# Performance work log

Hardware: AMD Instinct MI355X
Metric: run time of the kernel (lower is better)

Reference implementation:

```python
import jax, jax.numpy as jnp
import numpy as np

IN, H, OUT = 128, 256, 128


def setup_inputs() -> dict:
    key = jax.random.key(0)
    ks = jax.random.split(key, 12)
    B, T = 32, 128
    s_in = 1.0 / np.sqrt(IN)
    s_h = 1.0 / np.sqrt(H)
    return {
        "x": jax.random.normal(ks[0], (B, T, IN), dtype=jnp.float32),
        "timespans": jax.random.uniform(ks[1], (B, T), dtype=jnp.float32),
        "tau_sys": jax.random.uniform(ks[2], (H,), dtype=jnp.float32) * 10.0 + 1.0,
        "sigma": jnp.ones((H,), dtype=jnp.float32) * 0.5,
        "W_A": jax.random.normal(ks[3], (H, H), dtype=jnp.float32) * s_h,
        "W_B": jax.random.normal(ks[4], (H, IN), dtype=jnp.float32) * s_in,
        "b_B": jax.random.normal(ks[5], (H,), dtype=jnp.float32) * s_in,
        "W_C": jax.random.normal(ks[6], (OUT, H), dtype=jnp.float32) * s_h,
        "b_C": jax.random.normal(ks[7], (OUT,), dtype=jnp.float32) * s_h,
        "W_ih": jax.random.normal(ks[8], (4 * H, IN), dtype=jnp.float32) * s_h,
        "W_hh": jax.random.normal(ks[9], (4 * H, H), dtype=jnp.float32) * s_h,
        "b_ih": jax.random.normal(ks[10], (4 * H,), dtype=jnp.float32) * s_h,
        "b_hh": jax.random.normal(ks[11], (4 * H,), dtype=jnp.float32) * s_h,
    }


def _lstm(x, W_ih, W_hh, b_ih, b_hh):
    # x: [B,T,IN] -> backbone_out: [B,T,H]; torch gate order i,f,g,o
    B = x.shape[0]
    xg = jnp.einsum("bti,gi->btg", x, W_ih) + b_ih  # precompute input contribution

    def step(carry, xg_t):
        h, c = carry
        gates = xg_t + h @ W_hh.T + b_hh
        i, f, g, o = jnp.split(gates, 4, axis=-1)
        c = jax.nn.sigmoid(f) * c + jax.nn.sigmoid(i) * jnp.tanh(g)
        h = jax.nn.sigmoid(o) * jnp.tanh(c)
        return (h, c), h

    h0 = jnp.zeros((B, H), dtype=x.dtype)
    c0 = jnp.zeros((B, H), dtype=x.dtype)
    _, hs = jax.lax.scan(step, (h0, c0), jnp.swapaxes(xg, 0, 1))
    return jnp.swapaxes(hs, 0, 1)  # [B,T,H]


def reference(x, timespans, tau_sys, sigma, W_A, W_B, b_B, W_C, b_C,
              W_ih, W_hh, b_ih, b_hh):
    B, T, _ = x.shape
    backbone_out = _lstm(x, W_ih, W_hh, b_ih, b_hh)  # [B,T,H]

    A_eff = W_A / tau_sys[None, :]        # [H,H] (divide columns, as in torch)
    I = jnp.eye(H, dtype=x.dtype)
    Bx = jnp.einsum("bti,hi->bth", x, W_B) + b_B  # precompute B(x_t) for all t

    def step(h, inp):
        x_t_Bx, bb_t, ts_t = inp  # [B,H], [B,H], [B]
        f_h = jnp.tanh(h / sigma)
        At = A_eff[None, :, :] * ts_t[:, None, None]            # [B,H,H]
        exp_At = I + At + 0.5 * jnp.einsum("bij,bjk->bik", At, At)
        h_new = jnp.einsum("bij,bj->bi", exp_At, h)
        drive = x_t_Bx + f_h @ W_A.T
        h_new = h_new + ts_t[:, None] * drive / tau_sys[None, :]
        h_new = h_new + bb_t
        y = h_new @ W_C.T + b_C
        return h_new, y

    h0 = jnp.zeros((B, H), dtype=x.dtype)
    xs = (jnp.swapaxes(Bx, 0, 1), jnp.swapaxes(backbone_out, 0, 1),
          jnp.swapaxes(timespans, 0, 1))
    _, ys = jax.lax.scan(step, h0, xs)
    return jnp.swapaxes(ys, 0, 1)  # [B,T,OUT]
```

## Files before the change

### kernel.cpp

```cpp
#include <hip/hip_runtime.h>
#include <math.h>

#define T_ 128

#define OFF_M2      0
#define OFF_WCOMBT  65536
#define OFF_BIAS    229376
#define OFF_WCT     230656
#define OFF_XG2     263424
#define OFF_BX2     4457728
#define OFF_HSEQ    5506304
#define OFF_HCSEQ   6554880

#define SENTB 0xFFFFFFFFu

typedef float f4 __attribute__((ext_vector_type(4)));

__device__ __forceinline__ float sigm_f(float x) { return 1.0f / (1.0f + __expf(-x)); }
__device__ __forceinline__ float tanh_f(float x) { return 1.0f - 2.0f / (__expf(2.0f * x) + 1.0f); }

__device__ __forceinline__ unsigned long long aload_u64(const unsigned long long* p) {
  return __hip_atomic_load(p, __ATOMIC_RELAXED, __HIP_MEMORY_SCOPE_AGENT);
}
__device__ __forceinline__ void astore_f(float* p, float v) {
  __hip_atomic_store(p, v, __ATOMIC_RELAXED, __HIP_MEMORY_SCOPE_AGENT);
}
__device__ __forceinline__ bool bad_u64(unsigned long long v) {
  return (unsigned)v == SENTB || (unsigned)(v >> 32) == SENTB;
}

__global__ __launch_bounds__(256) void prep_kernel(
    const float* __restrict__ W_ih, const float* __restrict__ W_B,
    const float* __restrict__ b_ih, const float* __restrict__ b_hh,
    const float* __restrict__ b_B,  const float* __restrict__ W_C,
    const float* __restrict__ W_A,  const float* __restrict__ tau,
    float* __restrict__ ws) {
  __shared__ float adrow[256];
  const int blk = blockIdx.x, tid = threadIdx.x;
  if (blk < 640) {
    const int idx = blk * 256 + tid;
    const int k = idx / 1280, c = idx - k * 1280;
    ws[OFF_WCOMBT + idx] = (c < 1024) ? W_ih[c * 128 + k] : W_B[(c - 1024) * 128 + k];
  } else if (blk == 640) {
#pragma unroll
    for (int i = 0; i < 5; ++i) {
      const int id = i * 256 + tid;
      ws[OFF_BIAS + id] = (id < 1024) ? (b_ih[id] + b_hh[id]) : b_B[id - 1024];
    }
  } else if (blk < 769) {
    const int idx = (blk - 641) * 256 + tid;
    const int k = idx >> 7, o = idx & 127;
    ws[OFF_WCT + idx] = W_C[o * 256 + k];
  } else if (blk < 1025) {
    const int i = blk - 769, k = tid;
    const float itk = 1.0f / tau[k];
    adrow[k] = W_A[i * 256 + k] * itk;
    __syncthreads();
    float s = 0.f;
#pragma unroll 8
    for (int m = 0; m < 256; ++m)
      s = fmaf(adrow[m], W_A[m * 256 + k], s);
    ws[OFF_M2 + i * 256 + k] = s * itk;
  } else {
    uint4* dst = (uint4*)(ws + OFF_HSEQ);
    const uint4 sv = make_uint4(SENTB, SENTB, SENTB, SENTB);
    const int tg = (blk - 1025) * 256 + tid;
#pragma unroll
    for (int i = 0; i < 16; ++i) dst[tg + i * 32768] = sv;
  }
}

__global__ __launch_bounds__(256) void xgt_kernel(
    const float* __restrict__ x, const float* __restrict__ WT,
    const float* __restrict__ bias, float* __restrict__ xg2,
    float* __restrict__ bx2) {
  __shared__ float xs[32 * 128];
  const int tid = threadIdx.x;
  const int rt = blockIdx.x, ct = blockIdx.y;
  {
    const float4* src4 = (const float4*)(x + (size_t)rt * 4096);
    float4* d4 = (float4*)xs;
#pragma unroll
    for (int v = 0; v < 4; ++v) d4[v * 256 + tid] = src4[v * 256 + tid];
  }
  __syncthreads();
  const int rg = tid >> 5, cg = tid & 31;
  const int c0 = ct * 256 + cg * 8;
  const float4* b4 = (const float4*)(bias + c0);
  const float4 bA = b4[0], bB = b4[1];
  float a[4][8];
#pragma unroll
  for (int i = 0; i < 4; ++i) {
    a[i][0] = bA.x; a[i][1] = bA.y; a[i][2] = bA.z; a[i][3] = bA.w;
    a[i][4] = bB.x; a[i][5] = bB.y; a[i][6] = bB.z; a[i][7] = bB.w;
  }
  const float4* xr0 = (const float4*)(xs + (rg * 4 + 0) * 128);
  const float4* xr1 = (const float4*)(xs + (rg * 4 + 1) * 128);
  const float4* xr2 = (const float4*)(xs + (rg * 4 + 2) * 128);
  const float4* xr3 = (const float4*)(xs + (rg * 4 + 3) * 128);
#pragma unroll 2
  for (int k4 = 0; k4 < 32; ++k4) {
    const float4 xv0 = xr0[k4], xv1 = xr1[k4], xv2 = xr2[k4], xv3 = xr3[k4];
    const float xk[4][4] = {
        {xv0.x, xv0.y, xv0.z, xv0.w}, {xv1.x, xv1.y, xv1.z, xv1.w},
        {xv2.x, xv2.y, xv2.z, xv2.w}, {xv3.x, xv3.y, xv3.z, xv3.w}};
#pragma unroll
    for (int kk = 0; kk < 4; ++kk) {
      const float4* wp = (const float4*)(WT + (k4 * 4 + kk) * 1280 + c0);
      const float4 wA = wp[0], wB = wp[1];
      const float wv[8] = {wA.x, wA.y, wA.z, wA.w, wB.x, wB.y, wB.z, wB.w};
#pragma unroll
      for (int i = 0; i < 4; ++i)
#pragma unroll
        for (int j = 0; j < 8; ++j)
          a[i][j] = fmaf(wv[j], xk[i][kk], a[i][j]);
    }
  }
#pragma unroll
  for (int i = 0; i < 4; ++i) {
    const int row = rt * 32 + rg * 4 + i;
    const int b = row >> 7, t = row & 127;
    float* dst = (ct < 4)
        ? xg2 + (size_t)(t * 32 + b) * 1024 + ct * 256 + cg * 8
        : bx2 + (size_t)(t * 32 + b) * 256 + cg * 8;
    float4* d4 = (float4*)dst;
    d4[0] = make_float4(a[i][0], a[i][1], a[i][2], a[i][3]);
    d4[1] = make_float4(a[i][4], a[i][5], a[i][6], a[i][7]);
  }
}

__device__ __forceinline__ float wc_elem(
    const float* __restrict__ W_A, const float* __restrict__ M2,
    const float* __restrict__ tau, int ci, float it_i, int kp) {
  if (kp < 256)      return W_A[ci * 256 + kp] / tau[kp];
  else if (kp < 512) return W_A[ci * 256 + (kp - 256)] * it_i;
  else               return 0.5f * M2[ci * 256 + (kp - 512)];
}

__global__ __launch_bounds__(256, 4) void recur_bp_kernel(
    const float* __restrict__ ts_all, const float* __restrict__ tau,
    const float* __restrict__ sigma, const float* __restrict__ W_hh,
    const float* __restrict__ W_A, const float* __restrict__ M2,
    const float* __restrict__ xg2, const float* __restrict__ bx2,
    float* __restrict__ hseq, float* __restrict__ hcseq,
    const float* __restrict__ WCT, const float* __restrict__ bC,
    float* __restrict__ y) {
  const int tid = threadIdx.x;
  const int lane = tid & 63, w = tid >> 6;
  const unsigned long long* hsq  = (const unsigned long long*)hseq;
  const unsigned long long* hcsq = (const unsigned long long*)hcseq;

  __shared__ float h_s[2][256];
  __shared__ float q_s[2][768];

  if (blockIdx.x < 512) {
    const int b = blockIdx.x >> 4, cb16 = blockIdx.x & 15;
    const int kq = lane & 3;
    const int gt = (lane >> 2) & 3;
    const int dim = cb16 * 16 + 4 * w + (lane >> 4);
    const int grow = gt * 256 + dim;
    const f4* wsrc = (const f4*)(W_hh + grow * 256);
    f4 wq0  = wsrc[0 * 4 + kq],  wq1  = wsrc[1 * 4 + kq];
    f4 wq2  = wsrc[2 * 4 + kq],  wq3  = wsrc[3 * 4 + kq];
    f4 wq4  = wsrc[4 * 4 + kq],  wq5  = wsrc[5 * 4 + kq];
    f4 wq6  = wsrc[6 * 4 + kq],  wq7  = wsrc[7 * 4 + kq];
    f4 wq8  = wsrc[8 * 4 + kq],  wq9  = wsrc[9 * 4 + kq];
    f4 wq10 = wsrc[10 * 4 + kq], wq11 = wsrc[11 * 4 + kq];
    f4 wq12 = wsrc[12 * 4 + kq], wq13 = wsrc[13 * 4 + kq];
    f4 wq14 = wsrc[14 * 4 + kq], wq15 = wsrc[15 * 4 + kq];
    asm volatile("" : "+v"(wq0), "+v"(wq1), "+v"(wq2), "+v"(wq3),
                      "+v"(wq4), "+v"(wq5), "+v"(wq6), "+v"(wq7),
                      "+v"(wq8), "+v"(wq9), "+v"(wq10), "+v"(wq11),
                      "+v"(wq12), "+v"(wq13), "+v"(wq14), "+v"(wq15));
    float c_reg = 0.f;
    const int dcol = dim;

    for (int t = 0; t < T_; ++t) {
      const int buf = t & 1;
      float xgi = 0.f, xgf = 0.f, xgg = 0.f, xgo = 0.f;
      if ((lane & 15) == 0) {
        const float* xp = xg2 + (size_t)(t * 32 + b) * 1024 + dcol;
        xgi = xp[0]; xgf = xp[256]; xgg = xp[512]; xgo = xp[768];
      }
      if (t == 0) {
        if (tid < 128) ((float2*)h_s[0])[tid] = make_float2(0.f, 0.f);
      } else if (tid < 128) {
        const unsigned long long* pp = hsq + (size_t)((t - 1) * 32 + b) * 128 + tid;
        unsigned long long v = aload_u64(pp);
        int spins = 0;
        while (bad_u64(v)) {
          if (++spins > 16) __builtin_amdgcn_s_sleep(1);
          v = aload_u64(pp);
        }
        union { unsigned long long u; float2 f; } H; H.u = v;
        ((float2*)h_s[buf])[tid] = H.f;
      }
      __syncthreads();

      const f4* h4 = (const f4*)h_s[buf];
      float s = 0.f;
#define LSTEP(i4, W)                                                         \
      {                                                                      \
        const f4 hv = h4[i4 * 4 + kq];                                       \
        s = fmaf(W.x, hv.x, s); s = fmaf(W.y, hv.y, s);                      \
        s = fmaf(W.z, hv.z, s); s = fmaf(W.w, hv.w, s);                      \
      }
      LSTEP(0, wq0)   LSTEP(1, wq1)   LSTEP(2, wq2)   LSTEP(3, wq3)
      LSTEP(4, wq4)   LSTEP(5, wq5)   LSTEP(6, wq6)   LSTEP(7, wq7)
      LSTEP(8, wq8)   LSTEP(9, wq9)   LSTEP(10, wq10) LSTEP(11, wq11)
      LSTEP(12, wq12) LSTEP(13, wq13) LSTEP(14, wq14) LSTEP(15, wq15)
#undef LSTEP
      s += __shfl_xor(s, 1); s += __shfl_xor(s, 2);
      const int base = lane & 48;
      const float gi = __shfl(s, base);
      const float gf = __shfl(s, base + 4);
      const float gg = __shfl(s, base + 8);
      const float go = __shfl(s, base + 12);
      if ((lane & 15) == 0) {
        const float i_ = sigm_f(gi + xgi);
        const float f_ = sigm_f(gf + xgf);
        const float g_ = tanh_f(gg + xgg);
        const float o_ = sigm_f(go + xgo);
        c_reg = fmaf(f_, c_reg, i_ * g_);
        const float ht = o_ * tanh_f(c_reg);
        astore_f(hseq + (size_t)(t * 32 + b) * 256 + dcol, ht);
      }
      (void)gt;
    }
  } else {
    const int bix = blockIdx.x - 512;
    const int b = bix >> 4, cb16 = bix & 15;
    const int r_in = lane >> 4, kq16 = lane & 15;
    const int ci = cb16 * 16 + 4 * w + r_in;
    const float it_i = 1.0f / tau[ci];
#define WCLOAD(i4)                                                           \
    (f4){wc_elem(W_A, M2, tau, ci, it_i, (i4 * 16 + kq16) * 4 + 0),          \
         wc_elem(W_A, M2, tau, ci, it_i, (i4 * 16 + kq16) * 4 + 1),          \
         wc_elem(W_A, M2, tau, ci, it_i, (i4 * 16 + kq16) * 4 + 2),          \
         wc_elem(W_A, M2, tau, ci, it_i, (i4 * 16 + kq16) * 4 + 3)}
    f4 wc0  = WCLOAD(0),  wc1  = WCLOAD(1),  wc2  = WCLOAD(2);
    f4 wc3  = WCLOAD(3),  wc4  = WCLOAD(4),  wc5  = WCLOAD(5);
    f4 wc6  = WCLOAD(6),  wc7  = WCLOAD(7),  wc8  = WCLOAD(8);
    f4 wc9  = WCLOAD(9),  wc10 = WCLOAD(10), wc11 = WCLOAD(11);
#undef WCLOAD
    asm volatile("" : "+v"(wc0), "+v"(wc1), "+v"(wc2), "+v"(wc3),
                      "+v"(wc4), "+v"(wc5), "+v"(wc6), "+v"(wc7),
                      "+v"(wc8), "+v"(wc9), "+v"(wc10), "+v"(wc11));
    float2 isg2 = make_float2(0.f, 0.f);
    if (tid < 128) isg2 = make_float2(1.0f / sigma[2 * tid], 1.0f / sigma[2 * tid + 1]);
    const bool fin = (kq16 == 0);

    for (int t = 0; t < T_; ++t) {
      const int buf = t & 1;
      const float ts = ts_all[b * T_ + t];
      float bx_v = 0.f;
      if (fin) bx_v = bx2[(size_t)(t * 32 + b) * 256 + ci];

      if (t == 0) {
        if (tid < 128) {
          const float2 z = make_float2(0.f, 0.f);
          ((float2*)h_s[0])[tid] = z;
          float2* qrow = (float2*)q_s[0];
          qrow[tid] = z; qrow[128 + tid] = z; qrow[256 + tid] = z;
        }
      } else if (tid < 128) {
        const size_t base = (size_t)((t - 1) * 32 + b) * 128 + tid;
        const unsigned long long* pc = hcsq + base;
        const unsigned long long* ph = hsq + base;
        unsigned long long vc = aload_u64(pc);
        unsigned long long vh = aload_u64(ph);
        int spins = 0;
        while (bad_u64(vc) || bad_u64(vh)) {
          if (++spins > 16) __builtin_amdgcn_s_sleep(1);
          vc = aload_u64(pc);
          vh = aload_u64(ph);
        }
        union { unsigned long long u; float2 f; } C, H;
        C.u = vc; H.u = vh;
        const float2 hcv = make_float2(C.f.x + H.f.x, C.f.y + H.f.y);
        ((float2*)h_s[buf])[tid] = hcv;
        float2* qrow = (float2*)q_s[buf];
        qrow[tid]       = make_float2(ts * hcv.x, ts * hcv.y);
        qrow[128 + tid] = make_float2(ts * tanh_f(hcv.x * isg2.x),
                                      ts * tanh_f(hcv.y * isg2.y));
        qrow[256 + tid] = make_float2(ts * (ts * hcv.x), ts * (ts * hcv.y));
      }
      __syncthreads();

      const f4* q4 = (const f4*)q_s[buf];
      float s = 0.f;
#define CSTEP(i4, W)                                                         \
      {                                                                      \
        const f4 qv = q4[i4 * 16 + kq16];                                    \
        s = fmaf(W.x, qv.x, s); s = fmaf(W.y, qv.y, s);                      \
        s = fmaf(W.z, qv.z, s); s = fmaf(W.w, qv.w, s);                      \
      }
      CSTEP(0, wc0)  CSTEP(1, wc1)  CSTEP(2, wc2)  CSTEP(3, wc3)
      CSTEP(4, wc4)  CSTEP(5, wc5)  CSTEP(6, wc6)  CSTEP(7, wc7)
      CSTEP(8, wc8)  CSTEP(9, wc9)  CSTEP(10, wc10) CSTEP(11, wc11)
#undef CSTEP
      s += __shfl_xor(s, 1); s += __shfl_xor(s, 2);
      s += __shfl_xor(s, 4); s += __shfl_xor(s, 8);
      if (fin) {
        const float hc_own = h_s[buf][ci];
        const float hn_p = hc_own + s + ts * bx_v * it_i;
        astore_f(hcseq + (size_t)(t * 32 + b) * 256 + ci, hn_p);
      }
      (void)r_in;
    }
  }

  __syncthreads();
  {
    float* ys = &q_s[0][0];
    if (tid < 128) {
      size_t bases[4];
#pragma unroll
      for (int i = 0; i < 4; ++i) {
        const int row = 4 * (int)blockIdx.x + i;
        const int bb = row >> 7, tt = row & 127;
        bases[i] = (size_t)(tt * 32 + bb) * 128 + tid;
      }
      unsigned long long vc[4], vh[4];
      bool again; int spins = 0;
      do {
        again = false;
#pragma unroll
        for (int i = 0; i < 4; ++i) {
          vc[i] = aload_u64(hcsq + bases[i]);
          vh[i] = aload_u64(hsq + bases[i]);
        }
#pragma unroll
        for (int i = 0; i < 4; ++i)
          if (bad_u64(vc[i]) || bad_u64(vh[i])) again = true;
        if (again && ++spins > 16) __builtin_amdgcn_s_sleep(1);
      } while (again);
#pragma unroll
      for (int i = 0; i < 4; ++i) {
        union { unsigned long long u; float2 f; } C, H;
        C.u = vc[i]; H.u = vh[i];
        ((float2*)(ys + i * 256))[tid] =
            make_float2(C.f.x + H.f.x, C.f.y + H.f.y);
      }
    }
    __syncthreads();
    const int row = 4 * (int)blockIdx.x + w;
    const float2* bc2 = (const float2*)bC;
    float2 acc = bc2[lane];
    const float* yrow = ys + w * 256;
#pragma unroll 4
    for (int k = 0; k < 256; ++k) {
      const float hv = yrow[k];
      const float2 wv = ((const float2*)(WCT + k * 128))[lane];
      acc.x = fmaf(wv.x, hv, acc.x);
      acc.y = fmaf(wv.y, hv, acc.y);
    }
    ((float2*)(y + (size_t)row * 128))[lane] = acc;
  }
}

extern "C" void kernel_launch(void* const* d_in, const int* in_sizes, int n_in,
                              void* d_out, int out_size, void* d_ws, size_t ws_size,
                              hipStream_t stream) {
  const float* x     = (const float*)d_in[0];
  const float* tspan = (const float*)d_in[1];
  const float* tau   = (const float*)d_in[2];
  const float* sigma = (const float*)d_in[3];
  const float* W_A   = (const float*)d_in[4];
  const float* W_B   = (const float*)d_in[5];
  const float* b_B   = (const float*)d_in[6];
  const float* W_C   = (const float*)d_in[7];
  const float* b_C   = (const float*)d_in[8];
  const float* W_ih  = (const float*)d_in[9];
  const float* W_hh  = (const float*)d_in[10];
  const float* b_ih  = (const float*)d_in[11];
  const float* b_hh  = (const float*)d_in[12];
  float* ws = (float*)d_ws;
  float* y = (float*)d_out;

  prep_kernel<<<1153, 256, 0, stream>>>(W_ih, W_B, b_ih, b_hh, b_B, W_C,
                                        W_A, tau, ws);
  xgt_kernel<<<dim3(128, 5), 256, 0, stream>>>(x, ws + OFF_WCOMBT, ws + OFF_BIAS,
                                               ws + OFF_XG2, ws + OFF_BX2);
  recur_bp_kernel<<<1024, 256, 0, stream>>>(
      tspan, tau, sigma, W_hh, W_A, ws + OFF_M2, ws + OFF_XG2, ws + OFF_BX2,
      ws + OFF_HSEQ, ws + OFF_HCSEQ, ws + OFF_WCT, b_C, y);
}
```

Before: 368.9 us.

## Interleave LSTM gate preactivations and stage output weights through shared memory

The input-projection kernel now writes the four LSTM gate preactivations interleaved per hidden unit, so the recurrent loop fetches them with one 16-byte load instead of four strided scalar loads. The stores in the projection become strided scalar writes instead of float4 writes. The output-projection epilogue also stages W_C^T in 16-row chunks in shared memory, with block-wide barriers, instead of reading it from global memory per k. This adds 12 KB of shared memory per block, which may lower occupancy of the persistent recurrent kernel.

After: 448.2 us. +21.5%, slower.

```diff
diff --git a/kernel.cpp b/kernel.cpp
--- a/kernel.cpp
+++ b/kernel.cpp
@@ -120,12 +120,15 @@
   for (int i = 0; i < 4; ++i) {
     const int row = rt * 32 + rg * 4 + i;
     const int b = row >> 7, t = row & 127;
-    float* dst = (ct < 4)
-        ? xg2 + (size_t)(t * 32 + b) * 1024 + ct * 256 + cg * 8
-        : bx2 + (size_t)(t * 32 + b) * 256 + cg * 8;
-    float4* d4 = (float4*)dst;
-    d4[0] = make_float4(a[i][0], a[i][1], a[i][2], a[i][3]);
-    d4[1] = make_float4(a[i][4], a[i][5], a[i][6], a[i][7]);
+    if (ct < 4) {
+      float* dst = xg2 + (((size_t)(t * 32 + b) * 256 + cg * 8) * 4 + ct);
+#pragma unroll
+      for (int j = 0; j < 8; ++j) dst[j * 4] = a[i][j];
+    } else {
+      float4* d4 = (float4*)(bx2 + (size_t)(t * 32 + b) * 256 + cg * 8);
+      d4[0] = make_float4(a[i][0], a[i][1], a[i][2], a[i][3]);
+      d4[1] = make_float4(a[i][4], a[i][5], a[i][6], a[i][7]);
+    }
   }
 }
 
@@ -152,6 +155,8 @@
 
   __shared__ float h_s[2][256];
   __shared__ float q_s[2][768];
+  __shared__ float ys_s[1024];
+  __shared__ float wct_s[2048];
 
   if (blockIdx.x < 512) {
     const int b = blockIdx.x >> 4, cb16 = blockIdx.x & 15;
@@ -177,11 +182,9 @@
 
     for (int t = 0; t < T_; ++t) {
       const int buf = t & 1;
-      float xgi = 0.f, xgf = 0.f, xgg = 0.f, xgo = 0.f;
-      if ((lane & 15) == 0) {
-        const float* xp = xg2 + (size_t)(t * 32 + b) * 1024 + dcol;
-        xgi = xp[0]; xgf = xp[256]; xgg = xp[512]; xgo = xp[768];
-      }
+      f4 xgv = {0.f, 0.f, 0.f, 0.f};
+      if ((lane & 15) == 0)
+        xgv = *(const f4*)(xg2 + ((size_t)(t * 32 + b) * 256 + dcol) * 4);
       if (t == 0) {
         if (tid < 128) ((float2*)h_s[0])[tid] = make_float2(0.f, 0.f);
       } else if (tid < 128) {
@@ -217,10 +220,10 @@
       const float gg = __shfl(s, base + 8);
       const float go = __shfl(s, base + 12);
       if ((lane & 15) == 0) {
-        const float i_ = sigm_f(gi + xgi);
-        const float f_ = sigm_f(gf + xgf);
-        const float g_ = tanh_f(gg + xgg);
-        const float o_ = sigm_f(go + xgo);
+        const float i_ = sigm_f(gi + xgv.x);
+        const float f_ = sigm_f(gf + xgv.y);
+        const float g_ = tanh_f(gg + xgv.z);
+        const float o_ = sigm_f(go + xgv.w);
         c_reg = fmaf(f_, c_reg, i_ * g_);
         const float ht = o_ * tanh_f(c_reg);
         astore_f(hseq + (size_t)(t * 32 + b) * 256 + dcol, ht);
@@ -312,7 +315,6 @@
 
   __syncthreads();
   {
-    float* ys = &q_s[0][0];
     if (tid < 128) {
       size_t bases[4];
 #pragma unroll
@@ -339,21 +341,26 @@
       for (int i = 0; i < 4; ++i) {
         union { unsigned long long u; float2 f; } C, H;
         C.u = vc[i]; H.u = vh[i];
-        ((float2*)(ys + i * 256))[tid] =
+        ((float2*)(ys_s + i * 256))[tid] =
             make_float2(C.f.x + H.f.x, C.f.y + H.f.y);
       }
     }
     __syncthreads();
     const int row = 4 * (int)blockIdx.x + w;
-    const float2* bc2 = (const float2*)bC;
-    float2 acc = bc2[lane];
-    const float* yrow = ys + w * 256;
-#pragma unroll 4
-    for (int k = 0; k < 256; ++k) {
-      const float hv = yrow[k];
-      const float2 wv = ((const float2*)(WCT + k * 128))[lane];
-      acc.x = fmaf(wv.x, hv, acc.x);
-      acc.y = fmaf(wv.y, hv, acc.y);
+    float2 acc = ((const float2*)bC)[lane];
+    const float4* wct4 = (const float4*)WCT;
+    for (int chunk = 0; chunk < 16; ++chunk) {
+      ((float4*)wct_s)[2 * tid]     = wct4[chunk * 512 + 2 * tid];
+      ((float4*)wct_s)[2 * tid + 1] = wct4[chunk * 512 + 2 * tid + 1];
+      __syncthreads();
+#pragma unroll
+      for (int kk = 0; kk < 16; ++kk) {
+        const float hv = ys_s[w * 256 + chunk * 16 + kk];
+        const float2 wv = ((const float2*)wct_s)[kk * 64 + lane];
+        acc.x = fmaf(wv.x, hv, acc.x);
+        acc.y = fmaf(wv.y, hv, acc.y);
+      }
+      __syncthreads();
     }
     ((float2*)(y + (size_t)row * 128))[lane] = acc;
   }
```
